# Kernel optimization log

Hardware: AMD Instinct MI355X
Metric: run time of the kernel (lower is better)

Reference implementation:

```python
import jax, jax.numpy as jnp
import numpy as np

B, T = 8, 512
ACT, EMB, DET, HID, NST = 32, 1024, 1024, 1024, 16
STO, CLS = 32, 32
UNIMIX = 0.01


def _ln(x, g, b):
    m = x.mean(-1, keepdims=True)
    v = x.var(-1, keepdims=True)
    return (x - m) / jnp.sqrt(v + 1e-5) * g + b


def _lnsilu(x, g, b):
    return jax.nn.silu(_ln(x, g, b))


def setup_inputs() -> dict:
    key = jax.random.key(0)
    ks = iter(jax.random.split(key, 40))

    def lin(din, dout):
        return jax.random.normal(next(ks), (din, dout), jnp.float32) / np.sqrt(din)

    actions = jax.random.normal(next(ks), (B, T, ACT), jnp.float32)
    embeds = jax.random.normal(next(ks), (B, T, EMB), jnp.float32)
    # pre_ssm: Linear(ACT,HID) + LayerNormSiLU(HID)
    W_pre, b_pre = lin(ACT, HID), jnp.zeros(HID)
    g_pre, bb_pre = jnp.ones(HID), jnp.zeros(HID)
    W_emb = lin(EMB, HID)  # bias=False
    W_in, b_in = lin(HID, 2 * DET), jnp.zeros(2 * DET)
    W_dt = lin(DET, DET)
    # dt bias init: inverse-softplus of dt ~ LogUniform(1e-3, 0.1)
    u = jax.random.uniform(next(ks), (DET,), jnp.float32)
    dt_init = jnp.exp(u * (np.log(0.1) - np.log(1e-3)) + np.log(1e-3))
    b_dt = dt_init + jnp.log(-jnp.expm1(-dt_init))
    W_B, W_C = lin(DET, NST), lin(DET, NST)
    A_log = jnp.broadcast_to(
        jnp.log(jnp.arange(1, NST + 1, dtype=jnp.float32)), (DET, NST)
    ) + jnp.zeros((DET, NST))
    Dp = jnp.ones(DET)
    g_out, b_out = jnp.ones(DET), jnp.zeros(DET)
    # prior_net: Linear(DET,HID)+LNSiLU+Linear(HID,STO*CLS)
    W_pr1, b_pr1 = lin(DET, HID), jnp.zeros(HID)
    g_pr, bb_pr = jnp.ones(HID), jnp.zeros(HID)
    W_pr2, b_pr2 = lin(HID, STO * CLS), jnp.zeros(STO * CLS)
    # post_net: Linear(DET+EMB,HID)+LNSiLU+Linear(HID,STO*CLS)
    W_po1, b_po1 = lin(DET + EMB, HID), jnp.zeros(HID)
    g_po, bb_po = jnp.ones(HID), jnp.zeros(HID)
    W_po2, b_po2 = lin(HID, STO * CLS), jnp.zeros(STO * CLS)
    return dict(actions=actions, embeds=embeds, W_pre=W_pre, b_pre=b_pre,
                g_pre=g_pre, bb_pre=bb_pre, W_emb=W_emb, W_in=W_in, b_in=b_in,
                W_dt=W_dt, b_dt=b_dt, W_B=W_B, W_C=W_C, A_log=A_log, Dp=Dp,
                g_out=g_out, b_out=b_out, W_pr1=W_pr1, b_pr1=b_pr1, g_pr=g_pr,
                bb_pr=bb_pr, W_pr2=W_pr2, b_pr2=b_pr2, W_po1=W_po1, b_po1=b_po1,
                g_po=g_po, bb_po=bb_po, W_po2=W_po2, b_po2=b_po2)


def reference(actions, embeds, W_pre, b_pre, g_pre, bb_pre, W_emb, W_in, b_in,
              W_dt, b_dt, W_B, W_C, A_log, Dp, g_out, b_out, W_pr1, b_pr1,
              g_pr, bb_pr, W_pr2, b_pr2, W_po1, b_po1, g_po, bb_po, W_po2, b_po2):
    # input projections
    x = _lnsilu(actions @ W_pre + b_pre, g_pre, bb_pre) + embeds @ W_emb  # (B,T,HID)
    x = x.transpose(1, 0, 2)  # (T,B,HID)
    xz = x @ W_in + b_in
    x_ssm, x_gate = xz[..., :DET], xz[..., DET:]
    dt = jax.nn.softplus(x_ssm @ W_dt + b_dt)        # (T,B,DET)
    Bp = x_ssm @ W_B                                  # (T,B,NST)
    Cp = x_ssm @ W_C                                  # (T,B,NST)
    A = -jnp.exp(A_log)                               # (DET,NST)
    gates = jnp.exp(dt[..., None] * A)                # (T,B,DET,NST)
    values = (dt * x_ssm)[..., None] * Bp[:, :, None, :]

    # linear recurrence h[t] = g[t]*h[t-1] + v[t] via associative scan
    def comb(a, c):
        g1, v1 = a
        g2, v2 = c
        return (g1 * g2, g2 * v1 + v2)

    _, h = jax.lax.associative_scan(comb, (gates, values), axis=0)
    y = jnp.einsum('tbdn,tbn->tbd', h, Cp) + Dp * x_ssm
    y = y * jax.nn.silu(x_gate)
    deter = _ln(y, g_out, b_out)                      # (T,B,DET)

    # prior / post heads
    prior = _lnsilu(deter @ W_pr1 + b_pr1, g_pr, bb_pr) @ W_pr2 + b_pr2
    emb_t = embeds.transpose(1, 0, 2)
    post_in = jnp.concatenate([deter, emb_t], -1)
    post = _lnsilu(post_in @ W_po1 + b_po1, g_po, bb_po) @ W_po2 + b_po2
    # unimix transform of post logits (deterministic part of _categorical)
    p = jax.nn.softmax(post.reshape(T, B, STO, CLS), -1)
    p = (1.0 - UNIMIX) * p + UNIMIX / CLS
    post_u = jnp.log(p + 1e-8).reshape(T, B, STO * CLS)
    return jnp.concatenate([deter, prior, post_u], -1)  # (T,B,DET+2*STO*CLS)
```

## Files before the change

kernel.cpp:

```cpp
#include <hip/hip_runtime.h>
#include <hip/hip_bf16.h>
#include <math.h>


typedef __bf16 bf16_t;
typedef __bf16 bf16x8 __attribute__((ext_vector_type(8)));
typedef float f32x4 __attribute__((ext_vector_type(4)));

#define B_   8
#define T_   512
#define R_   4096
#define HID_ 1024
#define NC_  32
#define CL_  16

static __device__ __forceinline__ float bf2f(bf16_t x) { return (float)x; }
static __device__ __forceinline__ bf16_t f2bf(float x) { return (bf16_t)x; }
static __device__ __forceinline__ float ldany(const void* p, size_t i, bool isb) {
  return isb ? bf2f(((const bf16_t*)p)[i]) : ((const float*)p)[i];
}

typedef __attribute__((address_space(3))) unsigned int lds_u32;
typedef const __attribute__((address_space(1))) unsigned int glb_u32;
static __device__ __forceinline__ void gld16(const bf16_t* g, bf16_t* l) {
  __builtin_amdgcn_global_load_lds((glb_u32*)g, (lds_u32*)l, 16, 0, 0);
}

__global__ void detect_k(const unsigned int* __restrict__ dp_raw, int* __restrict__ flag) {
  if (threadIdx.x == 0) *flag = (dp_raw[0] == 0x3F803F80u) ? 1 : 0;
}

struct CvtArgs {
  const void* src[17];
  float* dst[17];
  int n[17];
};
__global__ __launch_bounds__(256) void cvt_vecs(CvtArgs a, const int* __restrict__ flag) {
  const bool isb = (*flag != 0);
  int v = blockIdx.y;
  const void* s = a.src[v];
  float* d = a.dst[v];
  int n = a.n[v];
  for (int i = blockIdx.x * 256 + threadIdx.x; i < n; i += 8 * 256)
    d[i] = ldany(s, i, isb);
}

__device__ __forceinline__ void block_sum2(float& s, float& ss) {
#pragma unroll
  for (int off = 32; off > 0; off >>= 1) {
    s  += __shfl_down(s, off, 64);
    ss += __shfl_down(ss, off, 64);
  }
  __shared__ float red[8];
  int tid = threadIdx.x;
  int wave = tid >> 6, lane = tid & 63;
  if (lane == 0) { red[wave] = s; red[4 + wave] = ss; }
  __syncthreads();
  s  = red[0] + red[1] + red[2] + red[3];
  ss = red[4] + red[5] + red[6] + red[7];
}

struct TrArgs {
  const void* src[8];
  bf16_t* dst[8];
  int K[8], N[8];
  int tile0[9];
};
__global__ void tr_batch(TrArgs a, const int* __restrict__ flag) {
  __shared__ float tile[32][33];
  const bool isb = (*flag != 0);
  int bid = blockIdx.x;
  int m = 0;
#pragma unroll
  for (int q = 0; q < 7; ++q) if (bid >= a.tile0[q + 1]) m = q + 1;
  int local = bid - a.tile0[m];
  int K = a.K[m], N = a.N[m];
  int ntx = N >> 5;
  int n0 = (local % ntx) * 32, k0 = (local / ntx) * 32;
  const void* src = a.src[m];
  bf16_t* dst = a.dst[m];
  int tx = threadIdx.x, ty = threadIdx.y;
#pragma unroll
  for (int i = 0; i < 4; ++i) {
    size_t idx = (size_t)(k0 + ty + i * 8) * N + n0 + tx;
    tile[ty + i * 8][tx] = ldany(src, idx, isb);
  }
  __syncthreads();
#pragma unroll
  for (int i = 0; i < 4; ++i)
    dst[(size_t)(n0 + ty + i * 8) * K + k0 + tx] = f2bf(tile[tx][ty + i * 8]);
}

__global__ __launch_bounds__(256) void prep_misc(const void* __restrict__ emb,
                                                 bf16_t* __restrict__ embT,
                                                 const void* __restrict__ W_B,
                                                 const void* __restrict__ W_C,
                                                 bf16_t* __restrict__ WTdtbc,
                                                 const int* __restrict__ flag) {
  const bool isb = (*flag != 0);
  int bid = blockIdx.x, tid = threadIdx.x;
  if (bid < 4096) {
    int r = bid;
    int t = r >> 3, b = r & 7;
    size_t base = (size_t)(b * T_ + t) * 1024;
#pragma unroll
    for (int i = 0; i < 4; ++i) {
      int c = i * 256 + tid;
      embT[(size_t)r * 1024 + c] = f2bf(ldany(emb, base + c, isb));
    }
  } else {
    int idx = (bid - 4096) * 256 + tid;
    int r = idx >> 10, k = idx & 1023;
    float v = 0.f;
    if (r < 16)      v = ldany(W_B, k * 16 + r, isb);
    else if (r < 32) v = ldany(W_C, k * 16 + (r - 16), isb);
    WTdtbc[(size_t)(1024 + r) * 1024 + k] = f2bf(v);
  }
}

__global__ __launch_bounds__(256) void preact_k(const void* __restrict__ act,
                                                const bf16_t* __restrict__ WTpre,
                                                const float* __restrict__ bias,
                                                const float* __restrict__ gw,
                                                const float* __restrict__ bw,
                                                bf16_t* __restrict__ out,
                                                const int* __restrict__ flag) {
  const bool isb = (*flag != 0);
  int r = blockIdx.x, tid = threadIdx.x;
  int t = r >> 3, b = r & 7;
  float av[32];
  size_t abase = (size_t)(b * T_ + t) * 32;
#pragma unroll
  for (int k = 0; k < 32; ++k) av[k] = bf2f(f2bf(ldany(act, abase + k, isb)));
  float v[4];
  float s = 0.f, ss = 0.f;
#pragma unroll
  for (int i = 0; i < 4; ++i) {
    int c = i * 256 + tid;
    const bf16x8* w8 = (const bf16x8*)(WTpre + (size_t)c * 32);
    float acc = 0.f;
#pragma unroll
    for (int q = 0; q < 4; ++q) {
      bf16x8 w = w8[q];
#pragma unroll
      for (int u = 0; u < 8; ++u) acc += av[q * 8 + u] * bf2f(w[u]);
    }
    v[i] = acc + bias[c];
    s += v[i]; ss += v[i] * v[i];
  }
  block_sum2(s, ss);
  float mean = s * (1.f / 1024.f);
  float var  = ss * (1.f / 1024.f) - mean * mean;
  float rstd = rsqrtf(var + 1e-5f);
#pragma unroll
  for (int i = 0; i < 4; ++i) {
    int c = i * 256 + tid;
    float yv = (v[i] - mean) * rstd * gw[c] + bw[c];
    yv = yv / (1.f + __expf(-yv));
    out[(size_t)r * 1024 + c] = f2bf(yv);
  }
}

enum { EPI_ADD_BF16 = 0, EPI_XZ = 1, EPI_BIAS_F32 = 3, EPI_PRIOR = 4,
       EPI_DTBC = 6, EPI_SMAX = 7 };

struct GemmArgs {
  const bf16_t* A;
  const bf16_t* Bt;
  int K;
  int N;
  int bnN;
  const float* bias;
  const bf16_t* addh;
  float* outf0;
  float* outf1;
  float* outf2;
  bf16_t* outh0;
  bf16_t* outh1;
  void* outv;
  const int* flag;
};

template <int EPI>
__device__ __forceinline__ void gemm_body(const GemmArgs& g, int idx,
                                          bf16_t* As, bf16_t* Bs) {
  const int tid = threadIdx.x;
  const int wave = tid >> 6, lane = tid & 63;
  const int K = g.K;
  const int bm = idx / g.bnN, bn = idx % g.bnN;

  f32x4 acc[2][2] = {};

  const int srow = tid >> 2;
  const int sblk = (tid & 3) ^ ((srow >> 1) & 3);
  const bf16_t* Ap = g.A  + (size_t)(bm * 64 + srow) * K + sblk * 8;
  const bf16_t* Bp = g.Bt + (size_t)(bn * 64 + srow) * K + sblk * 8;
  bf16_t* AsW = &As[tid * 8];
  bf16_t* BsW = &Bs[tid * 8];

  const int wm = (wave >> 1) * 32, wn = (wave & 1) * 32;
  const int fm = lane & 15;
  const int swz = (lane >> 4) ^ ((fm >> 1) & 3);

  for (int k0 = 0; k0 < K; k0 += 32) {
    gld16(Ap + k0, AsW);
    gld16(Bp + k0, BsW);
    __syncthreads();
    bf16x8 af[2], bfr[2];
#pragma unroll
    for (int i = 0; i < 2; ++i)
      af[i] = *(const bf16x8*)&As[((wm + i * 16 + fm) * 4 + swz) * 8];
#pragma unroll
    for (int j = 0; j < 2; ++j)
      bfr[j] = *(const bf16x8*)&Bs[((wn + j * 16 + fm) * 4 + swz) * 8];
#pragma unroll
    for (int i = 0; i < 2; ++i)
#pragma unroll
      for (int j = 0; j < 2; ++j)
        acc[i][j] = __builtin_amdgcn_mfma_f32_16x16x32_bf16(af[i], bfr[j], acc[i][j], 0, 0, 0);
    __syncthreads();
  }

  const int em = (lane >> 4) * 4, en = lane & 15;

  if constexpr (EPI == EPI_SMAX) {
    const bool ob = (*g.flag != 0);
#pragma unroll
    for (int i = 0; i < 2; ++i) {
#pragma unroll
      for (int v = 0; v < 4; ++v) {
        int row = bm * 64 + wm + i * 16 + em + v;
        int c0 = bn * 64 + wn + en;
        int c1 = c0 + 16;
        float x0 = acc[i][0][v] + g.bias[c0];
        float x1 = acc[i][1][v] + g.bias[c1];
        float m = fmaxf(x0, x1);
#pragma unroll
        for (int d = 1; d < 16; d <<= 1) m = fmaxf(m, __shfl_xor(m, d, 64));
        float e0 = __expf(x0 - m), e1 = __expf(x1 - m);
        float s = e0 + e1;
#pragma unroll
        for (int d = 1; d < 16; d <<= 1) s += __shfl_xor(s, d, 64);
        float inv = 0.99f / s;
        float p0 = logf(e0 * inv + (0.01f / 32.f) + 1e-8f);
        float p1 = logf(e1 * inv + (0.01f / 32.f) + 1e-8f);
        size_t o0 = (size_t)row * 3072 + 2048 + c0;
        if (ob) { ((bf16_t*)g.outv)[o0] = f2bf(p0); ((bf16_t*)g.outv)[o0 + 16] = f2bf(p1); }
        else    { ((float*)g.outv)[o0]  = p0;       ((float*)g.outv)[o0 + 16]  = p1; }
      }
    }
    return;
  }

  const bool out_bf = (EPI == EPI_PRIOR) ? (*g.flag != 0) : false;
#pragma unroll
  for (int i = 0; i < 2; ++i) {
#pragma unroll
    for (int j = 0; j < 2; ++j) {
#pragma unroll
      for (int v = 0; v < 4; ++v) {
        int row = bm * 64 + wm + i * 16 + em + v;
        int col = bn * 64 + wn + j * 16 + en;
        float x = acc[i][j][v];
        if constexpr (EPI == EPI_ADD_BF16) {
          size_t o = (size_t)row * g.N + col;
          g.outh0[o] = f2bf(x + bf2f(g.addh[o]));
        } else if constexpr (EPI == EPI_XZ) {
          float val = x + g.bias[col];
          if (col < 1024) g.outh0[(size_t)row * 1024 + col] = f2bf(val);
          else            g.outh1[(size_t)row * 1024 + (col - 1024)] = f2bf(val);
        } else if constexpr (EPI == EPI_BIAS_F32) {
          g.outf0[(size_t)row * g.N + col] = x + g.bias[col];
        } else if constexpr (EPI == EPI_DTBC) {
          if (col < 1024) {
            float val = x + g.bias[col];
            float sp = (val > 20.f) ? val : log1pf(__expf(val));
            g.outf0[(size_t)row * 1024 + col] = sp;
          } else if (col < 1040) {
            g.outf1[(size_t)row * 16 + (col - 1024)] = x;
          } else if (col < 1056) {
            g.outf2[(size_t)row * 16 + (col - 1040)] = x;
          }
        } else {
          float val = x + g.bias[col];
          size_t o = (size_t)row * 3072 + 1024 + col;
          if (out_bf) ((bf16_t*)g.outv)[o] = f2bf(val);
          else        ((float*)g.outv)[o]  = val;
        }
      }
    }
  }
}

template <int EPI>
__global__ __launch_bounds__(256) void gemm_t(GemmArgs g) {
  __shared__ __align__(16) bf16_t As[64 * 32];
  __shared__ __align__(16) bf16_t Bs[64 * 32];
  const int per = gridDim.x >> 3;
  const int idx = (blockIdx.x & 7) * per + (blockIdx.x >> 3);
  gemm_body<EPI>(g, idx, As, Bs);
}

struct GrpArgs { GemmArgs g0, g1; int tiles0; };
template <int E0, int E1>
__global__ __launch_bounds__(256) void gemm_g2(GrpArgs ga) {
  __shared__ __align__(16) bf16_t As[64 * 32];
  __shared__ __align__(16) bf16_t Bs[64 * 32];
  const int per = gridDim.x >> 3;
  const int half = per >> 1;
  const int xcd = blockIdx.x & 7;
  const int j = blockIdx.x >> 3;
  if (j < half) gemm_body<E0>(ga.g0, xcd * half + j, As, Bs);
  else          gemm_body<E1>(ga.g1, xcd * half + (j - half), As, Bs);
}

__global__ __launch_bounds__(256) void scan_p1(const float* __restrict__ dt,
                                               const bf16_t* __restrict__ xsh,
                                               const float* __restrict__ Bp,
                                               const float* __restrict__ A_log,
                                               float* __restrict__ Gp,
                                               float* __restrict__ Hl) {
  int idx = blockIdx.x * 256 + threadIdx.x;
  int d = idx & 1023;
  int cb = idx >> 10;
  int b = cb & 7, c = cb >> 3;
  float Ad[16];
#pragma unroll
  for (int n = 0; n < 16; ++n) Ad[n] = -__expf(A_log[d * 16 + n]);
  float h[16] = {};
  float dts = 0.f;
  int r0 = c * CL_ * 8 + b;
  for (int tl = 0; tl < CL_; ++tl) {
    int r = r0 + tl * 8;
    size_t off = (size_t)r * 1024 + d;
    float dtv = dt[off], xv = bf2f(xsh[off]);
    float dtx = dtv * xv;
    dts += dtv;
    const float4* Bp4 = (const float4*)(Bp + r * 16);
    float4 b4[4] = {Bp4[0], Bp4[1], Bp4[2], Bp4[3]};
    const float* bv = (const float*)b4;
#pragma unroll
    for (int n = 0; n < 16; ++n) {
      float gg = __expf(dtv * Ad[n]);
      h[n] = gg * h[n] + dtx * bv[n];
    }
  }
  float* gp = Gp + (size_t)idx * 16;
  float* hl = Hl + (size_t)idx * 16;
#pragma unroll
  for (int q = 0; q < 4; ++q) {
    float4 gq, hq;
    gq.x = __expf(dts * Ad[q * 4 + 0]); gq.y = __expf(dts * Ad[q * 4 + 1]);
    gq.z = __expf(dts * Ad[q * 4 + 2]); gq.w = __expf(dts * Ad[q * 4 + 3]);
    hq.x = h[q * 4 + 0]; hq.y = h[q * 4 + 1]; hq.z = h[q * 4 + 2]; hq.w = h[q * 4 + 3];
    ((float4*)gp)[q] = gq;
    ((float4*)hl)[q] = hq;
  }
}

__global__ __launch_bounds__(256) void scan_p2(float* __restrict__ GpCin,
                                               const float* __restrict__ Hl) {
  int j = blockIdx.x * 256 + threadIdx.x;
  float carry = 0.f;
#pragma unroll
  for (int c = 0; c < NC_; ++c) {
    size_t o = (size_t)c * 131072 + j;
    float gv = GpCin[o], hl = Hl[o];
    GpCin[o] = carry;
    carry = gv * carry + hl;
  }
}

__global__ __launch_bounds__(256) void scan_p3(const float* __restrict__ dt,
                                               const bf16_t* __restrict__ xsh,
                                               const bf16_t* __restrict__ xg,
                                               const float* __restrict__ Bp,
                                               const float* __restrict__ Cp,
                                               const float* __restrict__ A_log,
                                               const float* __restrict__ Dp,
                                               const float* __restrict__ Cin,
                                               float* __restrict__ y) {
  int idx = blockIdx.x * 256 + threadIdx.x;
  int d = idx & 1023;
  int cb = idx >> 10;
  int b = cb & 7, c = cb >> 3;
  float Ad[16];
#pragma unroll
  for (int n = 0; n < 16; ++n) Ad[n] = -__expf(A_log[d * 16 + n]);
  float Dd = Dp[d];
  float h[16];
  const float4* Ci4 = (const float4*)(Cin + (size_t)idx * 16);
#pragma unroll
  for (int q = 0; q < 4; ++q) {
    float4 cq = Ci4[q];
    h[q * 4 + 0] = cq.x; h[q * 4 + 1] = cq.y; h[q * 4 + 2] = cq.z; h[q * 4 + 3] = cq.w;
  }
  int r0 = c * CL_ * 8 + b;
  for (int tl = 0; tl < CL_; ++tl) {
    int r = r0 + tl * 8;
    size_t off = (size_t)r * 1024 + d;
    float dtv = dt[off], xv = bf2f(xsh[off]), gv = bf2f(xg[off]);
    float dtx = dtv * xv;
    const float4* Bp4 = (const float4*)(Bp + r * 16);
    const float4* Cp4 = (const float4*)(Cp + r * 16);
    float4 b4[4] = {Bp4[0], Bp4[1], Bp4[2], Bp4[3]};
    float4 c4[4] = {Cp4[0], Cp4[1], Cp4[2], Cp4[3]};
    const float* bv = (const float*)b4;
    const float* cv = (const float*)c4;
    float yv = 0.f;
#pragma unroll
    for (int n = 0; n < 16; ++n) {
      float gg = __expf(dtv * Ad[n]);
      h[n] = gg * h[n] + dtx * bv[n];
      yv += h[n] * cv[n];
    }
    yv += Dd * xv;
    float sg = gv / (1.f + __expf(-gv));
    y[off] = yv * sg;
  }
}

template <int MODE>
__global__ __launch_bounds__(256) void ln_k(const float* __restrict__ in,
                                            const float* __restrict__ gw,
                                            const float* __restrict__ bw,
                                            bf16_t* __restrict__ out0,
                                            void* __restrict__ out1,
                                            const bf16_t* __restrict__ embT,
                                            bf16_t* __restrict__ post_in,
                                            const int* __restrict__ flag) {
  const bool out_bf = (MODE == 0) ? (*flag != 0) : false;
  int r = blockIdx.x, tid = threadIdx.x;
  float v[4];
  float s = 0.f, ss = 0.f;
#pragma unroll
  for (int i = 0; i < 4; ++i) {
    v[i] = in[(size_t)r * 1024 + i * 256 + tid];
    s += v[i]; ss += v[i] * v[i];
  }
  block_sum2(s, ss);
  float mean = s * (1.f / 1024.f);
  float var  = ss * (1.f / 1024.f) - mean * mean;
  float rstd = rsqrtf(var + 1e-5f);
#pragma unroll
  for (int i = 0; i < 4; ++i) {
    int c = i * 256 + tid;
    float yv = (v[i] - mean) * rstd * gw[c] + bw[c];
    if constexpr (MODE == 1) yv = yv / (1.f + __expf(-yv));
    out0[(size_t)r * 1024 + c] = f2bf(yv);
    if constexpr (MODE == 0) {
      size_t o = (size_t)r * 3072 + c;
      if (out_bf) ((bf16_t*)out1)[o] = f2bf(yv);
      else        ((float*)out1)[o]  = yv;
      post_in[(size_t)r * 2048 + c] = f2bf(yv);
      post_in[(size_t)r * 2048 + 1024 + c] = embT[(size_t)r * 1024 + c];
    }
  }
}

__global__ __launch_bounds__(256) void ln2_k(const float* __restrict__ in0,
                                             const float* __restrict__ in1,
                                             const float* __restrict__ g0,
                                             const float* __restrict__ b0,
                                             const float* __restrict__ g1,
                                             const float* __restrict__ b1,
                                             bf16_t* __restrict__ o0,
                                             bf16_t* __restrict__ o1) {
  int r = blockIdx.x, tid = threadIdx.x;
  const float* in; const float* gw; const float* bw; bf16_t* out; int rr;
  if (r < 4096) { in = in0; gw = g0; bw = b0; out = o0; rr = r; }
  else          { in = in1; gw = g1; bw = b1; out = o1; rr = r - 4096; }
  float v[4];
  float s = 0.f, ss = 0.f;
#pragma unroll
  for (int i = 0; i < 4; ++i) {
    v[i] = in[(size_t)rr * 1024 + i * 256 + tid];
    s += v[i]; ss += v[i] * v[i];
  }
  block_sum2(s, ss);
  float mean = s * (1.f / 1024.f);
  float var  = ss * (1.f / 1024.f) - mean * mean;
  float rstd = rsqrtf(var + 1e-5f);
#pragma unroll
  for (int i = 0; i < 4; ++i) {
    int c = i * 256 + tid;
    float yv = (v[i] - mean) * rstd * gw[c] + bw[c];
    yv = yv / (1.f + __expf(-yv));
    out[(size_t)rr * 1024 + c] = f2bf(yv);
  }
}

extern "C" void kernel_launch(void* const* d_in, const int* in_sizes, int n_in,
                              void* d_out, int out_size, void* d_ws, size_t ws_size,
                              hipStream_t stream) {
  (void)in_sizes; (void)n_in; (void)out_size; (void)ws_size;
  const void* actions = d_in[0];
  const void* embeds  = d_in[1];
  const void* W_pre   = d_in[2];
  const void* b_pre   = d_in[3];
  const void* g_pre   = d_in[4];
  const void* bb_pre  = d_in[5];
  const void* W_emb   = d_in[6];
  const void* W_in    = d_in[7];
  const void* b_in    = d_in[8];
  const void* W_dt    = d_in[9];
  const void* b_dt    = d_in[10];
  const void* W_B     = d_in[11];
  const void* W_C     = d_in[12];
  const void* A_log   = d_in[13];
  const void* Dp      = d_in[14];
  const void* g_out   = d_in[15];
  const void* b_out   = d_in[16];
  const void* W_pr1   = d_in[17];
  const void* b_pr1   = d_in[18];
  const void* g_pr    = d_in[19];
  const void* bb_pr   = d_in[20];
  const void* W_pr2   = d_in[21];
  const void* b_pr2   = d_in[22];
  const void* W_po1   = d_in[23];
  const void* b_po1   = d_in[24];
  const void* g_po    = d_in[25];
  const void* bb_po   = d_in[26];
  const void* W_po2   = d_in[27];
  const void* b_po2   = d_in[28];

  char* ws = (char*)d_ws;
  const size_t KB = 1024;
  bf16_t* WTemb  = (bf16_t*)(ws + 0 * KB);
  bf16_t* WTin   = (bf16_t*)(ws + 2048 * KB);
  bf16_t* WTdtbc = (bf16_t*)(ws + 6144 * KB);
  bf16_t* WTpr1  = (bf16_t*)(ws + 8320 * KB);
  bf16_t* WTpr2  = (bf16_t*)(ws + 10368 * KB);
  bf16_t* WTpo1  = (bf16_t*)(ws + 12416 * KB);
  bf16_t* WTpo2  = (bf16_t*)(ws + 16512 * KB);
  bf16_t* embT   = (bf16_t*)(ws + 18560 * KB);
  float*  F1     = (float*)(ws + 26752 * KB);
  float*  F2     = (float*)(ws + 43136 * KB);
  float*  F5     = (float*)(ws + 59520 * KB);
  bf16_t* B8     = (bf16_t*)(ws + 75904 * KB);
  bf16_t* B9     = (bf16_t*)(ws + 84096 * KB);
  bf16_t* G8     = (bf16_t*)(ws + 92288 * KB);
  float*  BpB    = (float*)(ws + 100480 * KB);
  float*  CpB    = (float*)(ws + 100736 * KB);
  float*  Hl     = (float*)(ws + 59520 * KB);
  float*  Gp     = (float*)(ws + 43136 * KB);
  char* cb = ws + 100992 * KB;
  int*   flag    = (int*)(cb);                cb += 256;
  float* Alog_f  = (float*)(cb);              cb += 16384 * 4;
  float* Dp_f    = (float*)(cb);              cb += 1024 * 4;
  float* bpre_f  = (float*)(cb);              cb += 1024 * 4;
  float* gpre_f  = (float*)(cb);              cb += 1024 * 4;
  float* bbpre_f = (float*)(cb);              cb += 1024 * 4;
  float* bin_f   = (float*)(cb);              cb += 2048 * 4;
  float* bdt_f   = (float*)(cb);              cb += 1024 * 4;
  float* gout_f  = (float*)(cb);              cb += 1024 * 4;
  float* bout_f  = (float*)(cb);              cb += 1024 * 4;
  float* bpr1_f  = (float*)(cb);              cb += 1024 * 4;
  float* gpr_f   = (float*)(cb);              cb += 1024 * 4;
  float* bbpr_f  = (float*)(cb);              cb += 1024 * 4;
  float* bpr2_f  = (float*)(cb);              cb += 1024 * 4;
  float* bpo1_f  = (float*)(cb);              cb += 1024 * 4;
  float* gpo_f   = (float*)(cb);              cb += 1024 * 4;
  float* bbpo_f  = (float*)(cb);              cb += 1024 * 4;
  float* bpo2_f  = (float*)(cb);              cb += 1024 * 4;
  cb += 4096 * 32 * 2;
  bf16_t* WTpre  = (bf16_t*)(cb);             cb += 1024 * 32 * 2;

  detect_k<<<1, 64, 0, stream>>>((const unsigned int*)Dp, flag);

  CvtArgs ca{};
  const void* srcs[17] = {A_log, Dp, b_pre, g_pre, bb_pre, b_in, b_dt,
                          g_out, b_out, b_pr1, g_pr, bb_pr, b_pr2,
                          b_po1, g_po, bb_po, b_po2};
  float* dsts[17] = {Alog_f, Dp_f, bpre_f, gpre_f, bbpre_f, bin_f, bdt_f,
                     gout_f, bout_f, bpr1_f, gpr_f, bbpr_f, bpr2_f,
                     bpo1_f, gpo_f, bbpo_f, bpo2_f};
  int ns[17] = {16384, 1024, 1024, 1024, 1024, 2048, 1024,
                1024, 1024, 1024, 1024, 1024, 1024,
                1024, 1024, 1024, 1024};
  for (int i = 0; i < 17; ++i) { ca.src[i] = srcs[i]; ca.dst[i] = dsts[i]; ca.n[i] = ns[i]; }
  cvt_vecs<<<dim3(8, 17), 256, 0, stream>>>(ca, flag);

  {
    TrArgs ta{};
    const void* tsrc[8] = {W_emb, W_in, W_dt, W_pr1, W_pr2, W_po1, W_po2, W_pre};
    bf16_t* tdst[8] = {WTemb, WTin, WTdtbc, WTpr1, WTpr2, WTpo1, WTpo2, WTpre};
    int tK[8] = {1024, 1024, 1024, 1024, 1024, 2048, 1024, 32};
    int tN[8] = {1024, 2048, 1024, 1024, 1024, 1024, 1024, 1024};
    int off = 0;
    for (int i = 0; i < 8; ++i) {
      ta.src[i] = tsrc[i]; ta.dst[i] = tdst[i]; ta.K[i] = tK[i]; ta.N[i] = tN[i];
      ta.tile0[i] = off; off += (tK[i] >> 5) * (tN[i] >> 5);
    }
    ta.tile0[8] = off;
    tr_batch<<<off, dim3(32, 8), 0, stream>>>(ta, flag);
  }
  prep_misc<<<4352, 256, 0, stream>>>(embeds, embT, W_B, W_C, WTdtbc, flag);

  preact_k<<<R_, 256, 0, stream>>>(actions, WTpre, bpre_f, gpre_f, bbpre_f,
                                   B8, flag);
  {
    GemmArgs a{}; a.A = embT; a.Bt = WTemb; a.K = 1024; a.N = 1024; a.bnN = 16;
    a.addh = B8; a.outh0 = G8;
    gemm_t<EPI_ADD_BF16><<<1024, 256, 0, stream>>>(a);
  }
  {
    GemmArgs a{}; a.A = G8; a.Bt = WTin; a.K = 1024; a.N = 2048; a.bnN = 32;
    a.bias = bin_f; a.outh0 = B9; a.outh1 = B8;
    gemm_t<EPI_XZ><<<2048, 256, 0, stream>>>(a);
  }
  {
    GemmArgs a{}; a.A = B9; a.Bt = WTdtbc; a.K = 1024; a.N = 1088; a.bnN = 17;
    a.bias = bdt_f; a.outf0 = F1; a.outf1 = BpB; a.outf2 = CpB;
    gemm_t<EPI_DTBC><<<1088, 256, 0, stream>>>(a);
  }
  scan_p1<<<1024, 256, 0, stream>>>(F1, B9, BpB, Alog_f, Gp, Hl);
  scan_p2<<<512, 256, 0, stream>>>(Gp, Hl);
  scan_p3<<<1024, 256, 0, stream>>>(F1, B9, B8, BpB, CpB, Alog_f, Dp_f, Gp, F5);
  ln_k<0><<<R_, 256, 0, stream>>>(F5, gout_f, bout_f, B9, d_out,
                                  embT, (bf16_t*)F5, flag);
  {
    GrpArgs ga{};
    ga.g0.A = B9;            ga.g0.Bt = WTpr1; ga.g0.K = 1024; ga.g0.N = 1024;
    ga.g0.bnN = 16;          ga.g0.bias = bpr1_f; ga.g0.outf0 = F1;
    ga.g1.A = (bf16_t*)F5;   ga.g1.Bt = WTpo1; ga.g1.K = 2048; ga.g1.N = 1024;
    ga.g1.bnN = 16;          ga.g1.bias = bpo1_f; ga.g1.outf0 = F2;
    ga.tiles0 = 1024;
    gemm_g2<EPI_BIAS_F32, EPI_BIAS_F32><<<2048, 256, 0, stream>>>(ga);
  }
  ln2_k<<<2 * R_, 256, 0, stream>>>(F1, F2, gpr_f, bbpr_f, gpo_f, bbpo_f, B8, G8);
  {
    GrpArgs ga{};
    ga.g0.A = B8; ga.g0.Bt = WTpr2; ga.g0.K = 1024; ga.g0.N = 1024;
    ga.g0.bnN = 16; ga.g0.bias = bpr2_f; ga.g0.outv = d_out; ga.g0.flag = flag;
    ga.g1.A = G8; ga.g1.Bt = WTpo2; ga.g1.K = 1024; ga.g1.N = 1024;
    ga.g1.bnN = 16; ga.g1.bias = bpo2_f; ga.g1.outv = d_out; ga.g1.flag = flag;
    ga.tiles0 = 1024;
    gemm_g2<EPI_PRIOR, EPI_SMAX><<<2048, 256, 0, stream>>>(ga);
  }
}
```

Measured before the change: 470.4 us.

## Merge prep kernels into one launch and fuse output LayerNorm into scan pass

The flag detection, vector conversion, weight transposes, embedding/B-C packing and pre-activation kernels are merged into one multi-role prep launch. The pre-activation branch now reads W_pre and its LN vectors directly from the raw inputs instead of a transposed copy. The third scan pass becomes a 1024-thread block per (chunk, batch) that holds its 16 timesteps of y in registers and does the output LayerNorm in-block. This removes the fp32 y round trip through global memory and a separate LN launch. The cost is fewer, larger blocks (256 × 1024 threads), which may lower latency hiding in the scan. The pre-activation also loads weights with strided scalar reads instead of vectorised bf16 loads.

```diff
diff --git a/kernel.cpp b/kernel.cpp
--- a/kernel.cpp
+++ b/kernel.cpp
@@ -24,25 +24,6 @@
 typedef const __attribute__((address_space(1))) unsigned int glb_u32;
 static __device__ __forceinline__ void gld16(const bf16_t* g, bf16_t* l) {
   __builtin_amdgcn_global_load_lds((glb_u32*)g, (lds_u32*)l, 16, 0, 0);
-}
-
-__global__ void detect_k(const unsigned int* __restrict__ dp_raw, int* __restrict__ flag) {
-  if (threadIdx.x == 0) *flag = (dp_raw[0] == 0x3F803F80u) ? 1 : 0;
-}
-
-struct CvtArgs {
-  const void* src[17];
-  float* dst[17];
-  int n[17];
-};
-__global__ __launch_bounds__(256) void cvt_vecs(CvtArgs a, const int* __restrict__ flag) {
-  const bool isb = (*flag != 0);
-  int v = blockIdx.y;
-  const void* s = a.src[v];
-  float* d = a.dst[v];
-  int n = a.n[v];
-  for (int i = blockIdx.x * 256 + threadIdx.x; i < n; i += 8 * 256)
-    d[i] = ldany(s, i, isb);
 }
 
 __device__ __forceinline__ void block_sum2(float& s, float& ss) {
@@ -60,104 +41,103 @@
   ss = red[4] + red[5] + red[6] + red[7];
 }
 
-struct TrArgs {
-  const void* src[8];
-  bf16_t* dst[8];
-  int K[8], N[8];
-  int tile0[9];
+struct PrepArgs {
+  const void* csrc[17]; float* cdst[17]; int cn[17];
+  const void* tsrc[7]; bf16_t* tdst[7]; int tK[7], tN[7]; int tile0[8];
+  const void* emb; bf16_t* embT;
+  const void* W_B; const void* W_C; bf16_t* WTdtbc;
+  const void* act; const void* W_pre; const void* b_pre;
+  const void* g_pre; const void* bb_pre; bf16_t* preout;
+  const unsigned int* dp_raw; int* flag;
 };
-__global__ void tr_batch(TrArgs a, const int* __restrict__ flag) {
+__global__ __launch_bounds__(256) void prep_all(PrepArgs a) {
+  const bool isb = (a.dp_raw[0] == 0x3F803F80u);
+  const int bid = blockIdx.x, tid = threadIdx.x;
   __shared__ float tile[32][33];
-  const bool isb = (*flag != 0);
-  int bid = blockIdx.x;
-  int m = 0;
-#pragma unroll
-  for (int q = 0; q < 7; ++q) if (bid >= a.tile0[q + 1]) m = q + 1;
-  int local = bid - a.tile0[m];
-  int K = a.K[m], N = a.N[m];
-  int ntx = N >> 5;
-  int n0 = (local % ntx) * 32, k0 = (local / ntx) * 32;
-  const void* src = a.src[m];
-  bf16_t* dst = a.dst[m];
-  int tx = threadIdx.x, ty = threadIdx.y;
-#pragma unroll
-  for (int i = 0; i < 4; ++i) {
-    size_t idx = (size_t)(k0 + ty + i * 8) * N + n0 + tx;
-    tile[ty + i * 8][tx] = ldany(src, idx, isb);
-  }
-  __syncthreads();
-#pragma unroll
-  for (int i = 0; i < 4; ++i)
-    dst[(size_t)(n0 + ty + i * 8) * K + k0 + tx] = f2bf(tile[tx][ty + i * 8]);
-}
-
-__global__ __launch_bounds__(256) void prep_misc(const void* __restrict__ emb,
-                                                 bf16_t* __restrict__ embT,
-                                                 const void* __restrict__ W_B,
-                                                 const void* __restrict__ W_C,
-                                                 bf16_t* __restrict__ WTdtbc,
-                                                 const int* __restrict__ flag) {
-  const bool isb = (*flag != 0);
-  int bid = blockIdx.x, tid = threadIdx.x;
-  if (bid < 4096) {
-    int r = bid;
+  if (bid == 0) {
+    if (tid == 0) *a.flag = isb ? 1 : 0;
+    return;
+  }
+  if (bid < 137) {
+    int cv = bid - 1;
+    int v = cv >> 3;
+    const void* s = a.csrc[v]; float* dst = a.cdst[v]; int n = a.cn[v];
+    for (int i = (cv & 7) * 256 + tid; i < n; i += 2048) dst[i] = ldany(s, i, isb);
+    return;
+  }
+  if (bid < 9353) {
+    int tb = bid - 137;
+    int m = 0;
+#pragma unroll
+    for (int q = 0; q < 6; ++q) if (tb >= a.tile0[q + 1]) m = q + 1;
+    int local = tb - a.tile0[m];
+    int K = a.tK[m], N = a.tN[m];
+    int ntx = N >> 5;
+    int n0 = (local % ntx) * 32, k0 = (local / ntx) * 32;
+    const void* src = a.tsrc[m];
+    bf16_t* dst = a.tdst[m];
+    int tx = tid & 31, ty = tid >> 5;
+#pragma unroll
+    for (int i = 0; i < 4; ++i) {
+      size_t idx = (size_t)(k0 + ty + i * 8) * N + n0 + tx;
+      tile[ty + i * 8][tx] = ldany(src, idx, isb);
+    }
+    __syncthreads();
+#pragma unroll
+    for (int i = 0; i < 4; ++i)
+      dst[(size_t)(n0 + ty + i * 8) * K + k0 + tx] = f2bf(tile[tx][ty + i * 8]);
+    return;
+  }
+  if (bid < 13705) {
+    int mb = bid - 9353;
+    if (mb < 4096) {
+      int r = mb, t = r >> 3, b = r & 7;
+      size_t base = (size_t)(b * T_ + t) * 1024;
+#pragma unroll
+      for (int i = 0; i < 4; ++i) {
+        int c = i * 256 + tid;
+        a.embT[(size_t)r * 1024 + c] = f2bf(ldany(a.emb, base + c, isb));
+      }
+    } else {
+      int idx = (mb - 4096) * 256 + tid;
+      int r = idx >> 10, k = idx & 1023;
+      float v = 0.f;
+      if (r < 16)      v = ldany(a.W_B, k * 16 + r, isb);
+      else if (r < 32) v = ldany(a.W_C, k * 16 + (r - 16), isb);
+      a.WTdtbc[(size_t)(1024 + r) * 1024 + k] = f2bf(v);
+    }
+    return;
+  }
+  {
+    int r = bid - 13705;
     int t = r >> 3, b = r & 7;
-    size_t base = (size_t)(b * T_ + t) * 1024;
+    float av[32];
+    size_t abase = (size_t)(b * T_ + t) * 32;
+#pragma unroll
+    for (int k = 0; k < 32; ++k) av[k] = bf2f(f2bf(ldany(a.act, abase + k, isb)));
+    float v[4];
+    float s = 0.f, ss = 0.f;
 #pragma unroll
     for (int i = 0; i < 4; ++i) {
       int c = i * 256 + tid;
-      embT[(size_t)r * 1024 + c] = f2bf(ldany(emb, base + c, isb));
-    }
-  } else {
-    int idx = (bid - 4096) * 256 + tid;
-    int r = idx >> 10, k = idx & 1023;
-    float v = 0.f;
-    if (r < 16)      v = ldany(W_B, k * 16 + r, isb);
-    else if (r < 32) v = ldany(W_C, k * 16 + (r - 16), isb);
-    WTdtbc[(size_t)(1024 + r) * 1024 + k] = f2bf(v);
-  }
-}
-
-__global__ __launch_bounds__(256) void preact_k(const void* __restrict__ act,
-                                                const bf16_t* __restrict__ WTpre,
-                                                const float* __restrict__ bias,
-                                                const float* __restrict__ gw,
-                                                const float* __restrict__ bw,
-                                                bf16_t* __restrict__ out,
-                                                const int* __restrict__ flag) {
-  const bool isb = (*flag != 0);
-  int r = blockIdx.x, tid = threadIdx.x;
-  int t = r >> 3, b = r & 7;
-  float av[32];
-  size_t abase = (size_t)(b * T_ + t) * 32;
-#pragma unroll
-  for (int k = 0; k < 32; ++k) av[k] = bf2f(f2bf(ldany(act, abase + k, isb)));
-  float v[4];
-  float s = 0.f, ss = 0.f;
-#pragma unroll
-  for (int i = 0; i < 4; ++i) {
-    int c = i * 256 + tid;
-    const bf16x8* w8 = (const bf16x8*)(WTpre + (size_t)c * 32);
-    float acc = 0.f;
-#pragma unroll
-    for (int q = 0; q < 4; ++q) {
-      bf16x8 w = w8[q];
-#pragma unroll
-      for (int u = 0; u < 8; ++u) acc += av[q * 8 + u] * bf2f(w[u]);
-    }
-    v[i] = acc + bias[c];
-    s += v[i]; ss += v[i] * v[i];
-  }
-  block_sum2(s, ss);
-  float mean = s * (1.f / 1024.f);
-  float var  = ss * (1.f / 1024.f) - mean * mean;
-  float rstd = rsqrtf(var + 1e-5f);
-#pragma unroll
-  for (int i = 0; i < 4; ++i) {
-    int c = i * 256 + tid;
-    float yv = (v[i] - mean) * rstd * gw[c] + bw[c];
-    yv = yv / (1.f + __expf(-yv));
-    out[(size_t)r * 1024 + c] = f2bf(yv);
+      float acc = 0.f;
+#pragma unroll
+      for (int k = 0; k < 32; ++k)
+        acc += av[k] * bf2f(f2bf(ldany(a.W_pre, (size_t)k * 1024 + c, isb)));
+      v[i] = acc + ldany(a.b_pre, c, isb);
+      s += v[i]; ss += v[i] * v[i];
+    }
+    block_sum2(s, ss);
+    float mean = s * (1.f / 1024.f);
+    float var  = ss * (1.f / 1024.f) - mean * mean;
+    float rstd = rsqrtf(var + 1e-5f);
+#pragma unroll
+    for (int i = 0; i < 4; ++i) {
+      int c = i * 256 + tid;
+      float yv = (v[i] - mean) * rstd * ldany(a.g_pre, c, isb) + ldany(a.bb_pre, c, isb);
+      yv = yv / (1.f + __expf(-yv));
+      a.preout[(size_t)r * 1024 + c] = f2bf(yv);
+    }
   }
 }
 
@@ -371,31 +351,39 @@
   }
 }
 
-__global__ __launch_bounds__(256) void scan_p3(const float* __restrict__ dt,
-                                               const bf16_t* __restrict__ xsh,
-                                               const bf16_t* __restrict__ xg,
-                                               const float* __restrict__ Bp,
-                                               const float* __restrict__ Cp,
-                                               const float* __restrict__ A_log,
-                                               const float* __restrict__ Dp,
-                                               const float* __restrict__ Cin,
-                                               float* __restrict__ y) {
-  int idx = blockIdx.x * 256 + threadIdx.x;
-  int d = idx & 1023;
-  int cb = idx >> 10;
-  int b = cb & 7, c = cb >> 3;
+__global__ __launch_bounds__(1024) void scan_p3ln(const float* __restrict__ dt,
+                                                  const bf16_t* __restrict__ xsh,
+                                                  const bf16_t* __restrict__ xg,
+                                                  const float* __restrict__ Bp,
+                                                  const float* __restrict__ Cp,
+                                                  const float* __restrict__ A_log,
+                                                  const float* __restrict__ Dpv,
+                                                  const float* __restrict__ Cin,
+                                                  const float* __restrict__ gw,
+                                                  const float* __restrict__ bw,
+                                                  bf16_t* __restrict__ deter,
+                                                  void* __restrict__ dout,
+                                                  const bf16_t* __restrict__ embT,
+                                                  bf16_t* __restrict__ post_in,
+                                                  const int* __restrict__ flag) {
+  const bool out_bf = (*flag != 0);
+  const int cb = blockIdx.x;
+  const int b = cb & 7, c = cb >> 3;
+  const int d = threadIdx.x;
+  const int wave = d >> 6, lane = d & 63;
   float Ad[16];
 #pragma unroll
   for (int n = 0; n < 16; ++n) Ad[n] = -__expf(A_log[d * 16 + n]);
-  float Dd = Dp[d];
+  const float Dd = Dpv[d];
   float h[16];
-  const float4* Ci4 = (const float4*)(Cin + (size_t)idx * 16);
+  const float4* Ci4 = (const float4*)(Cin + ((size_t)cb * 1024 + d) * 16);
 #pragma unroll
   for (int q = 0; q < 4; ++q) {
     float4 cq = Ci4[q];
     h[q * 4 + 0] = cq.x; h[q * 4 + 1] = cq.y; h[q * 4 + 2] = cq.z; h[q * 4 + 3] = cq.w;
   }
-  int r0 = c * CL_ * 8 + b;
+  float yv16[16];
+  const int r0 = c * CL_ * 8 + b;
   for (int tl = 0; tl < CL_; ++tl) {
     int r = r0 + tl * 8;
     size_t off = (size_t)r * 1024 + d;
@@ -416,45 +404,49 @@
     }
     yv += Dd * xv;
     float sg = gv / (1.f + __expf(-gv));
-    y[off] = yv * sg;
-  }
-}
-
-template <int MODE>
-__global__ __launch_bounds__(256) void ln_k(const float* __restrict__ in,
-                                            const float* __restrict__ gw,
-                                            const float* __restrict__ bw,
-                                            bf16_t* __restrict__ out0,
-                                            void* __restrict__ out1,
-                                            const bf16_t* __restrict__ embT,
-                                            bf16_t* __restrict__ post_in,
-                                            const int* __restrict__ flag) {
-  const bool out_bf = (MODE == 0) ? (*flag != 0) : false;
-  int r = blockIdx.x, tid = threadIdx.x;
-  float v[4];
-  float s = 0.f, ss = 0.f;
-#pragma unroll
-  for (int i = 0; i < 4; ++i) {
-    v[i] = in[(size_t)r * 1024 + i * 256 + tid];
-    s += v[i]; ss += v[i] * v[i];
-  }
-  block_sum2(s, ss);
-  float mean = s * (1.f / 1024.f);
-  float var  = ss * (1.f / 1024.f) - mean * mean;
-  float rstd = rsqrtf(var + 1e-5f);
-#pragma unroll
-  for (int i = 0; i < 4; ++i) {
-    int c = i * 256 + tid;
-    float yv = (v[i] - mean) * rstd * gw[c] + bw[c];
-    if constexpr (MODE == 1) yv = yv / (1.f + __expf(-yv));
-    out0[(size_t)r * 1024 + c] = f2bf(yv);
-    if constexpr (MODE == 0) {
-      size_t o = (size_t)r * 3072 + c;
-      if (out_bf) ((bf16_t*)out1)[o] = f2bf(yv);
-      else        ((float*)out1)[o]  = yv;
-      post_in[(size_t)r * 2048 + c] = f2bf(yv);
-      post_in[(size_t)r * 2048 + 1024 + c] = embT[(size_t)r * 1024 + c];
-    }
+    yv16[tl] = yv * sg;
+  }
+  __shared__ float ls[16][17], lss[16][17];
+  __shared__ float lmean[16], lrstd[16];
+#pragma unroll
+  for (int tl = 0; tl < 16; ++tl) {
+    float s = yv16[tl], ss = yv16[tl] * yv16[tl];
+#pragma unroll
+    for (int o = 32; o > 0; o >>= 1) {
+      s  += __shfl_down(s, o, 64);
+      ss += __shfl_down(ss, o, 64);
+    }
+    if (lane == 0) { ls[tl][wave] = s; lss[tl][wave] = ss; }
+  }
+  __syncthreads();
+  {
+    float s  = (lane < 16) ? ls[wave][lane]  : 0.f;
+    float ss = (lane < 16) ? lss[wave][lane] : 0.f;
+#pragma unroll
+    for (int o = 8; o > 0; o >>= 1) {
+      s  += __shfl_down(s, o, 64);
+      ss += __shfl_down(ss, o, 64);
+    }
+    if (lane == 0) {
+      float mean = s * (1.f / 1024.f);
+      float var  = ss * (1.f / 1024.f) - mean * mean;
+      lmean[wave] = mean;
+      lrstd[wave] = rsqrtf(var + 1e-5f);
+    }
+  }
+  __syncthreads();
+  const float gwd = gw[d], bwd = bw[d];
+#pragma unroll
+  for (int tl = 0; tl < 16; ++tl) {
+    int r = r0 + tl * 8;
+    float yv = (yv16[tl] - lmean[tl]) * lrstd[tl] * gwd + bwd;
+    bf16_t yb = f2bf(yv);
+    deter[(size_t)r * 1024 + d] = yb;
+    size_t o = (size_t)r * 3072 + d;
+    if (out_bf) ((bf16_t*)dout)[o] = yb;
+    else        ((float*)dout)[o]  = yv;
+    post_in[(size_t)r * 2048 + d] = yb;
+    post_in[(size_t)r * 2048 + 1024 + d] = embT[(size_t)r * 1024 + d];
   }
 }
 
@@ -563,42 +555,37 @@
   float* gpo_f   = (float*)(cb);              cb += 1024 * 4;
   float* bbpo_f  = (float*)(cb);              cb += 1024 * 4;
   float* bpo2_f  = (float*)(cb);              cb += 1024 * 4;
-  cb += 4096 * 32 * 2;
-  bf16_t* WTpre  = (bf16_t*)(cb);             cb += 1024 * 32 * 2;
-
-  detect_k<<<1, 64, 0, stream>>>((const unsigned int*)Dp, flag);
-
-  CvtArgs ca{};
-  const void* srcs[17] = {A_log, Dp, b_pre, g_pre, bb_pre, b_in, b_dt,
-                          g_out, b_out, b_pr1, g_pr, bb_pr, b_pr2,
-                          b_po1, g_po, bb_po, b_po2};
-  float* dsts[17] = {Alog_f, Dp_f, bpre_f, gpre_f, bbpre_f, bin_f, bdt_f,
-                     gout_f, bout_f, bpr1_f, gpr_f, bbpr_f, bpr2_f,
-                     bpo1_f, gpo_f, bbpo_f, bpo2_f};
-  int ns[17] = {16384, 1024, 1024, 1024, 1024, 2048, 1024,
-                1024, 1024, 1024, 1024, 1024, 1024,
-                1024, 1024, 1024, 1024};
-  for (int i = 0; i < 17; ++i) { ca.src[i] = srcs[i]; ca.dst[i] = dsts[i]; ca.n[i] = ns[i]; }
-  cvt_vecs<<<dim3(8, 17), 256, 0, stream>>>(ca, flag);
-
-  {
-    TrArgs ta{};
-    const void* tsrc[8] = {W_emb, W_in, W_dt, W_pr1, W_pr2, W_po1, W_po2, W_pre};
-    bf16_t* tdst[8] = {WTemb, WTin, WTdtbc, WTpr1, WTpr2, WTpo1, WTpo2, WTpre};
-    int tK[8] = {1024, 1024, 1024, 1024, 1024, 2048, 1024, 32};
-    int tN[8] = {1024, 2048, 1024, 1024, 1024, 1024, 1024, 1024};
+
+  {
+    PrepArgs pa{};
+    const void* srcs[17] = {A_log, Dp, b_pre, g_pre, bb_pre, b_in, b_dt,
+                            g_out, b_out, b_pr1, g_pr, bb_pr, b_pr2,
+                            b_po1, g_po, bb_po, b_po2};
+    float* dsts[17] = {Alog_f, Dp_f, bpre_f, gpre_f, bbpre_f, bin_f, bdt_f,
+                       gout_f, bout_f, bpr1_f, gpr_f, bbpr_f, bpr2_f,
+                       bpo1_f, gpo_f, bbpo_f, bpo2_f};
+    int ns[17] = {16384, 1024, 1024, 1024, 1024, 2048, 1024,
+                  1024, 1024, 1024, 1024, 1024, 1024,
+                  1024, 1024, 1024, 1024};
+    for (int i = 0; i < 17; ++i) { pa.csrc[i] = srcs[i]; pa.cdst[i] = dsts[i]; pa.cn[i] = ns[i]; }
+    const void* tsrc[7] = {W_emb, W_in, W_dt, W_pr1, W_pr2, W_po1, W_po2};
+    bf16_t* tdst[7] = {WTemb, WTin, WTdtbc, WTpr1, WTpr2, WTpo1, WTpo2};
+    int tK[7] = {1024, 1024, 1024, 1024, 1024, 2048, 1024};
+    int tN[7] = {1024, 2048, 1024, 1024, 1024, 1024, 1024};
     int off = 0;
-    for (int i = 0; i < 8; ++i) {
-      ta.src[i] = tsrc[i]; ta.dst[i] = tdst[i]; ta.K[i] = tK[i]; ta.N[i] = tN[i];
-      ta.tile0[i] = off; off += (tK[i] >> 5) * (tN[i] >> 5);
-    }
-    ta.tile0[8] = off;
-    tr_batch<<<off, dim3(32, 8), 0, stream>>>(ta, flag);
-  }
-  prep_misc<<<4352, 256, 0, stream>>>(embeds, embT, W_B, W_C, WTdtbc, flag);
-
-  preact_k<<<R_, 256, 0, stream>>>(actions, WTpre, bpre_f, gpre_f, bbpre_f,
-                                   B8, flag);
+    for (int i = 0; i < 7; ++i) {
+      pa.tsrc[i] = tsrc[i]; pa.tdst[i] = tdst[i]; pa.tK[i] = tK[i]; pa.tN[i] = tN[i];
+      pa.tile0[i] = off; off += (tK[i] >> 5) * (tN[i] >> 5);
+    }
+    pa.tile0[7] = off;
+    pa.emb = embeds; pa.embT = embT;
+    pa.W_B = W_B; pa.W_C = W_C; pa.WTdtbc = WTdtbc;
+    pa.act = actions; pa.W_pre = W_pre; pa.b_pre = b_pre;
+    pa.g_pre = g_pre; pa.bb_pre = bb_pre; pa.preout = B8;
+    pa.dp_raw = (const unsigned int*)Dp; pa.flag = flag;
+    prep_all<<<17801, 256, 0, stream>>>(pa);
+  }
+
   {
     GemmArgs a{}; a.A = embT; a.Bt = WTemb; a.K = 1024; a.N = 1024; a.bnN = 16;
     a.addh = B8; a.outh0 = G8;
@@ -616,9 +603,9 @@
   }
   scan_p1<<<1024, 256, 0, stream>>>(F1, B9, BpB, Alog_f, Gp, Hl);
   scan_p2<<<512, 256, 0, stream>>>(Gp, Hl);
-  scan_p3<<<1024, 256, 0, stream>>>(F1, B9, B8, BpB, CpB, Alog_f, Dp_f, Gp, F5);
-  ln_k<0><<<R_, 256, 0, stream>>>(F5, gout_f, bout_f, B9, d_out,
-                                  embT, (bf16_t*)F5, flag);
+  scan_p3ln<<<256, 1024, 0, stream>>>(F1, B9, B8, BpB, CpB, Alog_f, Dp_f, Gp,
+                                      gout_f, bout_f, B9, d_out,
+                                      embT, (bf16_t*)F5, flag);
   {
     GrpArgs ga{};
     ga.g0.A = B9;            ga.g0.Bt = WTpr1; ga.g0.K = 1024; ga.g0.N = 1024;
```

Measured after the change: 609.6 us. 29.6% more time.

## Fuse scan phase 3 with output LayerNorm in one block per chunk-batch

Applied to the files above, without the earlier changes.

The separate scan_p3 and ln_k kernels become a single kernel. Each 1024-thread block owns one (chunk, batch) pair and keeps the 16 time-step outputs for all 1024 channels in registers. The LayerNorm statistics for those 16 rows are reduced through wave shuffles and shared memory, so the fp32 intermediate y no longer makes a round trip through global memory and one launch is dropped. In exchange the blocks are larger and hold more registers, there are two block-wide barriers, and an unused scratch offset is removed from the buffer carve-up.

```diff
diff --git a/kernel.cpp b/kernel.cpp
--- a/kernel.cpp
+++ b/kernel.cpp
@@ -371,31 +371,39 @@
   }
 }
 
-__global__ __launch_bounds__(256) void scan_p3(const float* __restrict__ dt,
-                                               const bf16_t* __restrict__ xsh,
-                                               const bf16_t* __restrict__ xg,
-                                               const float* __restrict__ Bp,
-                                               const float* __restrict__ Cp,
-                                               const float* __restrict__ A_log,
-                                               const float* __restrict__ Dp,
-                                               const float* __restrict__ Cin,
-                                               float* __restrict__ y) {
-  int idx = blockIdx.x * 256 + threadIdx.x;
-  int d = idx & 1023;
-  int cb = idx >> 10;
-  int b = cb & 7, c = cb >> 3;
+__global__ __launch_bounds__(1024) void scan_p3ln(const float* __restrict__ dt,
+                                                  const bf16_t* __restrict__ xsh,
+                                                  const bf16_t* __restrict__ xg,
+                                                  const float* __restrict__ Bp,
+                                                  const float* __restrict__ Cp,
+                                                  const float* __restrict__ A_log,
+                                                  const float* __restrict__ Dpv,
+                                                  const float* __restrict__ Cin,
+                                                  const float* __restrict__ gw,
+                                                  const float* __restrict__ bw,
+                                                  bf16_t* __restrict__ deter,
+                                                  void* __restrict__ dout,
+                                                  const bf16_t* __restrict__ embT,
+                                                  bf16_t* __restrict__ post_in,
+                                                  const int* __restrict__ flag) {
+  const bool out_bf = (*flag != 0);
+  const int cb = blockIdx.x;
+  const int b = cb & 7, c = cb >> 3;
+  const int d = threadIdx.x;
+  const int wave = d >> 6, lane = d & 63;
   float Ad[16];
 #pragma unroll
   for (int n = 0; n < 16; ++n) Ad[n] = -__expf(A_log[d * 16 + n]);
-  float Dd = Dp[d];
+  const float Dd = Dpv[d];
   float h[16];
-  const float4* Ci4 = (const float4*)(Cin + (size_t)idx * 16);
+  const float4* Ci4 = (const float4*)(Cin + ((size_t)cb * 1024 + d) * 16);
 #pragma unroll
   for (int q = 0; q < 4; ++q) {
     float4 cq = Ci4[q];
     h[q * 4 + 0] = cq.x; h[q * 4 + 1] = cq.y; h[q * 4 + 2] = cq.z; h[q * 4 + 3] = cq.w;
   }
-  int r0 = c * CL_ * 8 + b;
+  float yv16[16];
+  const int r0 = c * CL_ * 8 + b;
   for (int tl = 0; tl < CL_; ++tl) {
     int r = r0 + tl * 8;
     size_t off = (size_t)r * 1024 + d;
@@ -416,45 +424,49 @@
     }
     yv += Dd * xv;
     float sg = gv / (1.f + __expf(-gv));
-    y[off] = yv * sg;
-  }
-}
-
-template <int MODE>
-__global__ __launch_bounds__(256) void ln_k(const float* __restrict__ in,
-                                            const float* __restrict__ gw,
-                                            const float* __restrict__ bw,
-                                            bf16_t* __restrict__ out0,
-                                            void* __restrict__ out1,
-                                            const bf16_t* __restrict__ embT,
-                                            bf16_t* __restrict__ post_in,
-                                            const int* __restrict__ flag) {
-  const bool out_bf = (MODE == 0) ? (*flag != 0) : false;
-  int r = blockIdx.x, tid = threadIdx.x;
-  float v[4];
-  float s = 0.f, ss = 0.f;
-#pragma unroll
-  for (int i = 0; i < 4; ++i) {
-    v[i] = in[(size_t)r * 1024 + i * 256 + tid];
-    s += v[i]; ss += v[i] * v[i];
-  }
-  block_sum2(s, ss);
-  float mean = s * (1.f / 1024.f);
-  float var  = ss * (1.f / 1024.f) - mean * mean;
-  float rstd = rsqrtf(var + 1e-5f);
-#pragma unroll
-  for (int i = 0; i < 4; ++i) {
-    int c = i * 256 + tid;
-    float yv = (v[i] - mean) * rstd * gw[c] + bw[c];
-    if constexpr (MODE == 1) yv = yv / (1.f + __expf(-yv));
-    out0[(size_t)r * 1024 + c] = f2bf(yv);
-    if constexpr (MODE == 0) {
-      size_t o = (size_t)r * 3072 + c;
-      if (out_bf) ((bf16_t*)out1)[o] = f2bf(yv);
-      else        ((float*)out1)[o]  = yv;
-      post_in[(size_t)r * 2048 + c] = f2bf(yv);
-      post_in[(size_t)r * 2048 + 1024 + c] = embT[(size_t)r * 1024 + c];
-    }
+    yv16[tl] = yv * sg;
+  }
+  __shared__ float ls[16][17], lss[16][17];
+  __shared__ float lmean[16], lrstd[16];
+#pragma unroll
+  for (int tl = 0; tl < 16; ++tl) {
+    float s = yv16[tl], ss = yv16[tl] * yv16[tl];
+#pragma unroll
+    for (int o = 32; o > 0; o >>= 1) {
+      s  += __shfl_down(s, o, 64);
+      ss += __shfl_down(ss, o, 64);
+    }
+    if (lane == 0) { ls[tl][wave] = s; lss[tl][wave] = ss; }
+  }
+  __syncthreads();
+  {
+    float s  = (lane < 16) ? ls[wave][lane]  : 0.f;
+    float ss = (lane < 16) ? lss[wave][lane] : 0.f;
+#pragma unroll
+    for (int o = 8; o > 0; o >>= 1) {
+      s  += __shfl_down(s, o, 64);
+      ss += __shfl_down(ss, o, 64);
+    }
+    if (lane == 0) {
+      float mean = s * (1.f / 1024.f);
+      float var  = ss * (1.f / 1024.f) - mean * mean;
+      lmean[wave] = mean;
+      lrstd[wave] = rsqrtf(var + 1e-5f);
+    }
+  }
+  __syncthreads();
+  const float gwd = gw[d], bwd = bw[d];
+#pragma unroll
+  for (int tl = 0; tl < 16; ++tl) {
+    int r = r0 + tl * 8;
+    float yv = (yv16[tl] - lmean[tl]) * lrstd[tl] * gwd + bwd;
+    bf16_t yb = f2bf(yv);
+    deter[(size_t)r * 1024 + d] = yb;
+    size_t o = (size_t)r * 3072 + d;
+    if (out_bf) ((bf16_t*)dout)[o] = yb;
+    else        ((float*)dout)[o]  = yv;
+    post_in[(size_t)r * 2048 + d] = yb;
+    post_in[(size_t)r * 2048 + 1024 + d] = embT[(size_t)r * 1024 + d];
   }
 }
 
@@ -563,7 +575,6 @@
   float* gpo_f   = (float*)(cb);              cb += 1024 * 4;
   float* bbpo_f  = (float*)(cb);              cb += 1024 * 4;
   float* bpo2_f  = (float*)(cb);              cb += 1024 * 4;
-  cb += 4096 * 32 * 2;
   bf16_t* WTpre  = (bf16_t*)(cb);             cb += 1024 * 32 * 2;
 
   detect_k<<<1, 64, 0, stream>>>((const unsigned int*)Dp, flag);
@@ -616,9 +627,9 @@
   }
   scan_p1<<<1024, 256, 0, stream>>>(F1, B9, BpB, Alog_f, Gp, Hl);
   scan_p2<<<512, 256, 0, stream>>>(Gp, Hl);
-  scan_p3<<<1024, 256, 0, stream>>>(F1, B9, B8, BpB, CpB, Alog_f, Dp_f, Gp, F5);
-  ln_k<0><<<R_, 256, 0, stream>>>(F5, gout_f, bout_f, B9, d_out,
-                                  embT, (bf16_t*)F5, flag);
+  scan_p3ln<<<256, 1024, 0, stream>>>(F1, B9, B8, BpB, CpB, Alog_f, Dp_f, Gp,
+                                      gout_f, bout_f, B9, d_out,
+                                      embT, (bf16_t*)F5, flag);
   {
     GrpArgs ga{};
     ga.g0.A = B9;            ga.g0.Bt = WTpr1; ga.g0.K = 1024; ga.g0.N = 1024;
```

Measured after the change: 465.0 us. About the same (-1.1%).
